# Kernel optimization log

Measured on AMD Instinct MI355X. Metric: run time of the kernel, lower is better.

The kernel has to match this reference:

```python
import jax, jax.numpy as jnp
import numpy as np

B, M, N, E, H, HID = 4, 512, 512, 256, 16, 16
D = E // H


def setup_inputs() -> dict:
    key = jax.random.key(0)
    ks = jax.random.split(key, 10)
    u = lambda k, shape, lim: jax.random.uniform(k, shape, jnp.float32, -lim, lim)
    mix1_init = (1.0 / 2.0) ** 0.5
    mix2_init = (1.0 / 16.0) ** 0.5
    return {
        "q_input": jax.random.normal(ks[0], (B, M, E), jnp.float32),
        "kv_input": jax.random.normal(ks[1], (B, N, E), jnp.float32),
        "dmat": jax.random.uniform(ks[2], (B, M, N), jnp.float32),
        "Wq": u(ks[3], (E, E), 1.0 / np.sqrt(E)),
        "Wkv": u(ks[4], (2 * E, E), 1.0 / np.sqrt(E)),
        "mix_W1": u(ks[5], (H, 2, HID), mix1_init),
        "mix_b1": u(ks[6], (H, HID), mix1_init),
        "mix_W2": u(ks[7], (H, HID, 1), mix2_init),
        "mix_b2": u(ks[8], (H, 1), mix2_init),
        "Wout": u(ks[9], (E, E), 1.0 / np.sqrt(E)),
    }


def reference(q_input, kv_input, dmat, Wq, Wkv, mix_W1, mix_b1, mix_W2, mix_b2, Wout):
    b, m, e = q_input.shape
    n = kv_input.shape[1]
    h = mix_W1.shape[0]
    d = e // h
    # projections (torch Linear: y = x @ W.T)
    q = (q_input @ Wq.T).reshape(b, m, h, d).transpose(0, 2, 1, 3)        # b h m d
    kv = (kv_input @ Wkv.T).reshape(b, n, 2, h, d)                        # (two h d) split
    k = kv[:, :, 0].transpose(0, 2, 1, 3)                                 # b h n d
    v = kv[:, :, 1].transpose(0, 2, 1, 3)                                 # b h n d
    scale = jnp.sqrt(jnp.asarray(d, q.dtype))
    scores = jnp.einsum('bhmd,bhnd->bhmn', q, k) / scale                  # b h m n
    # mix scores with dmat via per-head 2-layer MLP on the last (size-2) axis
    mix = jnp.stack([scores, jnp.broadcast_to(dmat[:, None], scores.shape)], axis=-1)  # b h m n 2
    hidden = jax.nn.relu(jnp.einsum('bhmnt,htk->bhmnk', mix, mix_W1)
                         + mix_b1[None, :, None, None, :])                # b h m n HID
    mixed = (jnp.einsum('bhmnk,hko->bhmno', hidden, mix_W2)
             + mix_b2[None, :, None, None, :])[..., 0]                    # b h m n
    probs = jax.nn.softmax(mixed, axis=-1)
    out = jnp.einsum('bhmn,bhnd->bhmd', probs, v)                         # b h m d
    out = out.transpose(0, 2, 1, 3).reshape(b, m, e)                      # b m (h d)
    return out @ Wout.T
```

## Files before the change

kernel.cpp:

```cpp
#include <hip/hip_runtime.h>
#include <stdint.h>
#include <stddef.h>

#define MM 512
#define NN 512
#define EE 256
#define HH 16
#define DD 16

typedef __bf16 bf16x8 __attribute__((ext_vector_type(8)));
typedef float f32x4 __attribute__((ext_vector_type(4)));

static __device__ __forceinline__ bf16x8 bzero8() {
  bf16x8 z;
#pragma unroll
  for (int i = 0; i < 8; ++i) z[i] = (__bf16)0.0f;
  return z;
}

static __device__ __forceinline__ bf16x8 cvt8(const float* __restrict__ p) {
  const float4 u = *(const float4*)p;
  const float4 v = *(const float4*)(p + 4);
  bf16x8 r;
  r[0] = (__bf16)u.x; r[1] = (__bf16)u.y; r[2] = (__bf16)u.z; r[3] = (__bf16)u.w;
  r[4] = (__bf16)v.x; r[5] = (__bf16)v.y; r[6] = (__bf16)v.z; r[7] = (__bf16)v.w;
  return r;
}

static __device__ __forceinline__ unsigned short f2b(float f) {
  union { __bf16 h; unsigned short u; } cv;
  cv.h = (__bf16)f;
  return cv.u;
}

static __device__ __forceinline__ float b2f(unsigned short u) {
  union { unsigned int i; float f; } cv;
  cv.i = ((unsigned int)u) << 16;
  return cv.f;
}

static __device__ __forceinline__ float b2f_lo(unsigned int u) {
  return __int_as_float((int)(u << 16));
}
static __device__ __forceinline__ float b2f_hi(unsigned int u) {
  return __int_as_float((int)(u & 0xffff0000u));
}

static __device__ __forceinline__ float fexp2(float x) {
  float r;
  asm("v_exp_f32 %0, %1" : "=v"(r) : "v"(x));
  return r;
}

static __device__ __forceinline__ unsigned int cvtpk(float lo, float hi) {
  unsigned int r;
  asm("v_cvt_pk_bf16_f32 %0, %1, %2" : "=v"(r) : "v"(lo), "v"(hi));
  return r;
}

static __device__ __forceinline__ float sload(const float* p) {
  return __int_as_float(__builtin_amdgcn_readfirstlane(__float_as_int(*p)));
}

__global__ __launch_bounds__(256) void proj_all_kernel(
    const float* __restrict__ Xq, const float* __restrict__ Xkv,
    const float* __restrict__ Wq, const float* __restrict__ Wkv,
    const float* __restrict__ Wout, const float* __restrict__ dmat,
    unsigned short* __restrict__ Qs, unsigned short* __restrict__ Ks,
    unsigned short* __restrict__ Vt,
    unsigned short* __restrict__ Whi, unsigned short* __restrict__ Wlo,
    unsigned short* __restrict__ dmatb) {
  const int by = blockIdx.y;
  const int tid = threadIdx.x;

  if (by == 13) {
    const int base = blockIdx.x * 256 + tid;
#pragma unroll
    for (int it = 0; it < 16; ++it) {
      const int i4 = it * 16384 + base;
      const float4 v = *(const float4*)(dmat + (size_t)i4 * 4);
      uint2 u;
      u.x = cvtpk(v.x, v.y);
      u.y = cvtpk(v.z, v.w);
      *(uint2*)(dmatb + (size_t)i4 * 4) = u;
    }
    return;
  }

  if (by == 12) {
    const int base = (blockIdx.x * 256 + tid) * 4;
    const float4 v = *(const float4*)(Wout + base);
    float c4[4] = {v.x, v.y, v.z, v.w};
#pragma unroll
    for (int i = 0; i < 4; ++i) {
      const unsigned short hb = f2b(c4[i]);
      Whi[base + i] = hb;
      Wlo[base + i] = f2b(c4[i] - b2f(hb));
    }
    return;
  }

  const int w = tid >> 6, l = tid & 63;
  const int lg = l >> 4, lr = l & 15;
  const int t0 = blockIdx.x * 32 + (w & 1) * 16;

  if (by < 4) {
    const int n0 = by * 64 + (w >> 1) * 32;
    f32x4 acc0 = {0.f, 0.f, 0.f, 0.f}, acc1 = {0.f, 0.f, 0.f, 0.f};
#pragma unroll
    for (int kc = 0; kc < EE; kc += 32) {
      const int k = kc + lg * 8;
      bf16x8 a  = cvt8(Xq + (size_t)(t0 + lr) * EE + k);
      bf16x8 b0 = cvt8(Wq + (size_t)(n0 + lr) * EE + k);
      bf16x8 b1 = cvt8(Wq + (size_t)(n0 + 16 + lr) * EE + k);
      acc0 = __builtin_amdgcn_mfma_f32_16x16x32_bf16(a, b0, acc0, 0, 0, 0);
      acc1 = __builtin_amdgcn_mfma_f32_16x16x32_bf16(a, b1, acc1, 0, 0, 0);
    }
#pragma unroll
    for (int r = 0; r < 4; ++r) {
      const int t = t0 + 4 * lg + r, b = t >> 9, m = t & 511;
      const int j0 = n0 + lr, j1 = j0 + 16;
      Qs[((size_t)(b * HH + (j0 >> 4)) * MM + m) * DD + (j0 & 15)] = f2b(acc0[r] * 0.25f);
      Qs[((size_t)(b * HH + (j1 >> 4)) * MM + m) * DD + (j1 & 15)] = f2b(acc1[r] * 0.25f);
    }
  } else {
    const int n0 = (by - 4) * 64 + (w >> 1) * 32;
    f32x4 acc0 = {0.f, 0.f, 0.f, 0.f}, acc1 = {0.f, 0.f, 0.f, 0.f};
#pragma unroll
    for (int kc = 0; kc < EE; kc += 32) {
      const int k = kc + lg * 8;
      bf16x8 a  = cvt8(Xkv + (size_t)(t0 + lr) * EE + k);
      bf16x8 b0 = cvt8(Wkv + (size_t)(n0 + lr) * EE + k);
      bf16x8 b1 = cvt8(Wkv + (size_t)(n0 + 16 + lr) * EE + k);
      acc0 = __builtin_amdgcn_mfma_f32_16x16x32_bf16(a, b0, acc0, 0, 0, 0);
      acc1 = __builtin_amdgcn_mfma_f32_16x16x32_bf16(a, b1, acc1, 0, 0, 0);
    }
#pragma unroll
    for (int r = 0; r < 4; ++r) {
      const int t = t0 + 4 * lg + r, b = t >> 9, n = t & 511;
#pragma unroll
      for (int fi = 0; fi < 2; ++fi) {
        const int j = n0 + lr + fi * 16;
        const float v = fi ? acc1[r] : acc0[r];
        if (j < 256) {
          Ks[((size_t)(b * HH + (j >> 4)) * NN + n) * DD + (j & 15)] = f2b(v);
        } else {
          const int jj = j - 256;
          Vt[((size_t)(b * HH + (jj >> 4)) * DD + (jj & 15)) * NN + n] = f2b(v);
        }
      }
    }
  }
}

__global__ __launch_bounds__(256, 2) void attn_kernel(
    const unsigned short* __restrict__ Qs, const unsigned short* __restrict__ Ks,
    const unsigned short* __restrict__ Vt, const unsigned short* __restrict__ dmatb,
    const float* __restrict__ W1, const float* __restrict__ b1v,
    const float* __restrict__ W2,
    unsigned short* __restrict__ Ahi, unsigned short* __restrict__ Alo) {
  __shared__ unsigned short P[32][520];
  __shared__ float red[4][32];
  float (*pvred)[2][16][16] = (float (*)[2][16][16]) & P[0][0];

  const int tid = threadIdx.x, w = tid >> 6, l = tid & 63;
  const int lg = l >> 4, lr = l & 15;
  const int bid = blockIdx.x;
  const int xcd = bid & 7, slot = bid >> 3;
  const int hh = slot & 15;
  const int g = (slot >> 4) * 8 + xcd;
  const int b = g >> 4, mt = g & 15;
  const int m0 = mt * 32;
  const int n0 = w * 128;

  const unsigned short* Qbase = Qs + ((size_t)(b * HH + hh) * MM + m0) * DD;
  const unsigned short* Kbase = Ks + (size_t)(b * HH + hh) * NN * DD;
  const unsigned short* Vbase = Vt + (size_t)(b * HH + hh) * DD * NN;
  const unsigned short* dbase = dmatb + (size_t)b * MM * NN;

  float ckv[16], bkv[16], wkp[16];
  float Ac = 0.f, Cc = 0.f;
  const float hiln2 = 0.5f * 1.4426950408889634f;
#pragma unroll
  for (int k = 0; k < 16; ++k) {
    const float ak = sload(W1 + hh * 32 + k);
    const float ck = sload(W1 + hh * 32 + 16 + k);
    const float bk = sload(b1v + hh * 16 + k);
    const float wk = hiln2 * sload(W2 + hh * 16 + k);
    Ac += wk * ak;
    Cc += wk * ck;
    const float ra = 1.0f / ak;
    ckv[k] = ck * ra;
    bkv[k] = bk * ra;
    wkp[k] = wk * fabsf(ak);
    asm volatile("" : "+v"(ckv[k]));
    asm volatile("" : "+v"(bkv[k]));
  }

  bf16x8 qb[2];
#pragma unroll
  for (int mb = 0; mb < 2; ++mb) {
    qb[mb] = bzero8();
    if (lg < 2) qb[mb] = *(const bf16x8*)(Qbase + (mb * 16 + lr) * DD + lg * 8);
  }

  const f32x4 zf = {0.f, 0.f, 0.f, 0.f};
  float psum[2] = {0.f, 0.f};

  const unsigned short* dpl0 = dbase + (size_t)(m0 + lr) * NN + n0 + 4 * lg;
  const unsigned short* dpl1 = dbase + (size_t)(m0 + 16 + lr) * NN + n0 + 4 * lg;

  uint2 dva0 = *(const uint2*)(dpl0);
  uint2 dva1 = *(const uint2*)(dpl1);
  bf16x8 ka0 = bzero8();
  if (lg < 2) ka0 = *(const bf16x8*)(Kbase + (size_t)(n0 + lr) * DD + lg * 8);

#pragma unroll
  for (int nb = 0; nb < 8; ++nb) {
    uint2 dvb0, dvb1;
    bf16x8 ka1 = bzero8();
    if (nb < 7) {
      dvb0 = *(const uint2*)(dpl0 + (nb + 1) * 16);
      dvb1 = *(const uint2*)(dpl1 + (nb + 1) * 16);
      if (lg < 2)
        ka1 = *(const bf16x8*)(Kbase + (size_t)(n0 + (nb + 1) * 16 + lr) * DD + lg * 8);
    }

    f32x4 cc[2];
    cc[0] = __builtin_amdgcn_mfma_f32_16x16x32_bf16(ka0, qb[0], zf, 0, 0, 0);
    cc[1] = __builtin_amdgcn_mfma_f32_16x16x32_bf16(ka0, qb[1], zf, 0, 0, 0);

#pragma unroll
    for (int mb = 0; mb < 2; ++mb) {
      const uint2 dvv = mb ? dva1 : dva0;
      float dunp[4];
      dunp[0] = b2f_lo(dvv.x);
      dunp[1] = b2f_hi(dvv.x);
      dunp[2] = b2f_lo(dvv.y);
      dunp[3] = b2f_hi(dvv.y);
      float ev[4];
#pragma unroll
      for (int r = 0; r < 4; ++r) {
        const float s = cc[mb][r];
        const float d = dunp[r];
        float acc = fmaf(Ac, s, Cc * d);
#pragma unroll
        for (int k = 0; k < 16; ++k) {
          const float t = fmaf(ckv[k], d, bkv[k]);
          acc = fmaf(wkp[k], fabsf(s + t), acc);
        }
        const float e = fexp2(acc);
        psum[mb] += e;
        ev[r] = e;
      }
      uint2 u;
      u.x = cvtpk(ev[0], ev[1]);
      u.y = cvtpk(ev[2], ev[3]);
      *(uint2*)&P[mb * 16 + lr][n0 + nb * 16 + 4 * lg] = u;
    }

    dva0 = dvb0;
    dva1 = dvb1;
    ka0 = ka1;
  }

#pragma unroll
  for (int mb = 0; mb < 2; ++mb) {
    psum[mb] += __shfl_xor(psum[mb], 16);
    psum[mb] += __shfl_xor(psum[mb], 32);
    if (lg == 0) red[w][mb * 16 + lr] = psum[mb];
  }

  f32x4 pv[2];
  pv[0] = zf; pv[1] = zf;
#pragma unroll
  for (int kb = 0; kb < 4; ++kb) {
    const bf16x8 vb = *(const bf16x8*)(Vbase + (size_t)lr * NN + (n0 + kb * 32 + lg * 8));
#pragma unroll
    for (int mb = 0; mb < 2; ++mb) {
      const bf16x8 pa = *(const bf16x8*)(&P[mb * 16 + lr][n0 + kb * 32 + lg * 8]);
      pv[mb] = __builtin_amdgcn_mfma_f32_16x16x32_bf16(pa, vb, pv[mb], 0, 0, 0);
    }
  }
  __syncthreads();
#pragma unroll
  for (int mb = 0; mb < 2; ++mb)
#pragma unroll
    for (int r = 0; r < 4; ++r) pvred[w][mb][4 * lg + r][lr] = pv[mb][r];
  __syncthreads();

  for (int i = tid; i < 512; i += 256) {
    const int mr = i >> 4, dd = i & 15;
    const float s = pvred[0][mr >> 4][mr & 15][dd] + pvred[1][mr >> 4][mr & 15][dd] +
                    pvred[2][mr >> 4][mr & 15][dd] + pvred[3][mr >> 4][mr & 15][dd];
    const float rs = red[0][mr] + red[1][mr] + red[2][mr] + red[3][mr];
    const float val = s / rs;
    const unsigned short hb = f2b(val);
    const size_t o = ((size_t)(b * MM) + m0 + mr) * EE + hh * DD + dd;
    Ahi[o] = hb;
    Alo[o] = f2b(val - b2f(hb));
  }
}

__global__ __launch_bounds__(256) void out_gemm_kernel(
    const unsigned short* __restrict__ Ahi, const unsigned short* __restrict__ Alo,
    const unsigned short* __restrict__ Whi, const unsigned short* __restrict__ Wlo,
    float* __restrict__ out) {
  const int tid = threadIdx.x, w = tid >> 6, l = tid & 63;
  const int lg = l >> 4, lr = l & 15;
  const int t0 = blockIdx.x * 32 + (w & 1) * 16;
  const int n0 = blockIdx.y * 64 + (w >> 1) * 32;
  f32x4 acc0 = {0.f, 0.f, 0.f, 0.f}, acc1 = {0.f, 0.f, 0.f, 0.f};
#pragma unroll
  for (int kc = 0; kc < EE; kc += 32) {
    const int k = kc + lg * 8;
    const bf16x8 ah = *(const bf16x8*)(Ahi + (size_t)(t0 + lr) * EE + k);
    const bf16x8 al = *(const bf16x8*)(Alo + (size_t)(t0 + lr) * EE + k);
    const bf16x8 bh0 = *(const bf16x8*)(Whi + (size_t)(n0 + lr) * EE + k);
    const bf16x8 bh1 = *(const bf16x8*)(Whi + (size_t)(n0 + 16 + lr) * EE + k);
    const bf16x8 bl0 = *(const bf16x8*)(Wlo + (size_t)(n0 + lr) * EE + k);
    const bf16x8 bl1 = *(const bf16x8*)(Wlo + (size_t)(n0 + 16 + lr) * EE + k);
    acc0 = __builtin_amdgcn_mfma_f32_16x16x32_bf16(ah, bh0, acc0, 0, 0, 0);
    acc0 = __builtin_amdgcn_mfma_f32_16x16x32_bf16(al, bh0, acc0, 0, 0, 0);
    acc0 = __builtin_amdgcn_mfma_f32_16x16x32_bf16(ah, bl0, acc0, 0, 0, 0);
    acc1 = __builtin_amdgcn_mfma_f32_16x16x32_bf16(ah, bh1, acc1, 0, 0, 0);
    acc1 = __builtin_amdgcn_mfma_f32_16x16x32_bf16(al, bh1, acc1, 0, 0, 0);
    acc1 = __builtin_amdgcn_mfma_f32_16x16x32_bf16(ah, bl1, acc1, 0, 0, 0);
  }
#pragma unroll
  for (int r = 0; r < 4; ++r) {
    const int row = t0 + 4 * lg + r;
    out[(size_t)row * EE + n0 + lr] = acc0[r];
    out[(size_t)row * EE + n0 + 16 + lr] = acc1[r];
  }
}

extern "C" void kernel_launch(void* const* d_in, const int* in_sizes, int n_in,
                              void* d_out, int out_size, void* d_ws, size_t ws_size,
                              hipStream_t stream) {
  const float* q_input  = (const float*)d_in[0];
  const float* kv_input = (const float*)d_in[1];
  const float* dmat     = (const float*)d_in[2];
  const float* Wq       = (const float*)d_in[3];
  const float* Wkv      = (const float*)d_in[4];
  const float* W1       = (const float*)d_in[5];
  const float* b1       = (const float*)d_in[6];
  const float* W2       = (const float*)d_in[7];
  const float* Wout     = (const float*)d_in[9];
  float* out = (float*)d_out;

  char* ws = (char*)d_ws;
  unsigned short* Qs    = (unsigned short*)(ws);
  unsigned short* Ks    = (unsigned short*)(ws + (1u << 20));
  unsigned short* Vt    = (unsigned short*)(ws + (2u << 20));
  unsigned short* Ahi   = (unsigned short*)(ws + (3u << 20));
  unsigned short* Alo   = (unsigned short*)(ws + (4u << 20));
  unsigned short* Whi   = (unsigned short*)(ws + (5u << 20));
  unsigned short* Wlo   = (unsigned short*)(ws + (5u << 20) + (1u << 17));
  unsigned short* dmatb = (unsigned short*)(ws + (6u << 20));

  proj_all_kernel<<<dim3(64, 14), 256, 0, stream>>>(q_input, kv_input, Wq, Wkv, Wout,
                                                    dmat, Qs, Ks, Vt, Whi, Wlo, dmatb);
  attn_kernel<<<dim3(1024), 256, 0, stream>>>(Qs, Ks, Vt, dmatb, W1, b1, W2,
                                              Ahi, Alo);
  out_gemm_kernel<<<dim3(64, 4), 256, 0, stream>>>(Ahi, Alo, Whi, Wlo, out);
}
```

Measured before the change: 61.81 us.

## Fuse output projection into attention kernel with atomic accumulation

Removes the separate output GEMM kernel and the Ahi/Alo workspace round trip. Each attention block multiplies its 32x16 per-head tile against the matching 16-column slice of Wout and adds the partial result into the output with float atomics, which requires zeroing the output in the projection kernel first. This saves a kernel launch and global traffic but adds 16-way atomic contention per output element, K=16 MFMAs that are half-padded with zeros, and a nondeterministic summation order.

Result: slower. 77.47 us (+25.3%).

```diff
diff --git a/kernel.cpp b/kernel.cpp
--- a/kernel.cpp
+++ b/kernel.cpp
@@ -69,9 +69,18 @@
     unsigned short* __restrict__ Qs, unsigned short* __restrict__ Ks,
     unsigned short* __restrict__ Vt,
     unsigned short* __restrict__ Whi, unsigned short* __restrict__ Wlo,
-    unsigned short* __restrict__ dmatb) {
+    unsigned short* __restrict__ dmatb, float* __restrict__ out) {
   const int by = blockIdx.y;
   const int tid = threadIdx.x;
+
+  if (by == 14) {
+    const float4 z4 = {0.f, 0.f, 0.f, 0.f};
+    const int base = blockIdx.x * 256 + tid;
+#pragma unroll
+    for (int it = 0; it < 8; ++it)
+      *(float4*)(out + (size_t)(it * 16384 + base) * 4) = z4;
+    return;
+  }
 
   if (by == 13) {
     const int base = blockIdx.x * 256 + tid;
@@ -158,10 +167,13 @@
     const unsigned short* __restrict__ Vt, const unsigned short* __restrict__ dmatb,
     const float* __restrict__ W1, const float* __restrict__ b1v,
     const float* __restrict__ W2,
-    unsigned short* __restrict__ Ahi, unsigned short* __restrict__ Alo) {
+    const unsigned short* __restrict__ Whi, const unsigned short* __restrict__ Wlo,
+    float* __restrict__ out) {
   __shared__ unsigned short P[32][520];
   __shared__ float red[4][32];
   float (*pvred)[2][16][16] = (float (*)[2][16][16]) & P[0][0];
+  unsigned short (*A_lhi)[16] = (unsigned short (*)[16]) & P[20][0];
+  unsigned short (*A_llo)[16] = (unsigned short (*)[16]) & P[22][0];
 
   const int tid = threadIdx.x, w = tid >> 6, l = tid & 63;
   const int lg = l >> 4, lr = l & 15;
@@ -296,42 +308,39 @@
     const float rs = red[0][mr] + red[1][mr] + red[2][mr] + red[3][mr];
     const float val = s / rs;
     const unsigned short hb = f2b(val);
-    const size_t o = ((size_t)(b * MM) + m0 + mr) * EE + hh * DD + dd;
-    Ahi[o] = hb;
-    Alo[o] = f2b(val - b2f(hb));
-  }
-}
-
-__global__ __launch_bounds__(256) void out_gemm_kernel(
-    const unsigned short* __restrict__ Ahi, const unsigned short* __restrict__ Alo,
-    const unsigned short* __restrict__ Whi, const unsigned short* __restrict__ Wlo,
-    float* __restrict__ out) {
-  const int tid = threadIdx.x, w = tid >> 6, l = tid & 63;
-  const int lg = l >> 4, lr = l & 15;
-  const int t0 = blockIdx.x * 32 + (w & 1) * 16;
-  const int n0 = blockIdx.y * 64 + (w >> 1) * 32;
-  f32x4 acc0 = {0.f, 0.f, 0.f, 0.f}, acc1 = {0.f, 0.f, 0.f, 0.f};
-#pragma unroll
-  for (int kc = 0; kc < EE; kc += 32) {
-    const int k = kc + lg * 8;
-    const bf16x8 ah = *(const bf16x8*)(Ahi + (size_t)(t0 + lr) * EE + k);
-    const bf16x8 al = *(const bf16x8*)(Alo + (size_t)(t0 + lr) * EE + k);
-    const bf16x8 bh0 = *(const bf16x8*)(Whi + (size_t)(n0 + lr) * EE + k);
-    const bf16x8 bh1 = *(const bf16x8*)(Whi + (size_t)(n0 + 16 + lr) * EE + k);
-    const bf16x8 bl0 = *(const bf16x8*)(Wlo + (size_t)(n0 + lr) * EE + k);
-    const bf16x8 bl1 = *(const bf16x8*)(Wlo + (size_t)(n0 + 16 + lr) * EE + k);
-    acc0 = __builtin_amdgcn_mfma_f32_16x16x32_bf16(ah, bh0, acc0, 0, 0, 0);
-    acc0 = __builtin_amdgcn_mfma_f32_16x16x32_bf16(al, bh0, acc0, 0, 0, 0);
-    acc0 = __builtin_amdgcn_mfma_f32_16x16x32_bf16(ah, bl0, acc0, 0, 0, 0);
-    acc1 = __builtin_amdgcn_mfma_f32_16x16x32_bf16(ah, bh1, acc1, 0, 0, 0);
-    acc1 = __builtin_amdgcn_mfma_f32_16x16x32_bf16(al, bh1, acc1, 0, 0, 0);
-    acc1 = __builtin_amdgcn_mfma_f32_16x16x32_bf16(ah, bl1, acc1, 0, 0, 0);
-  }
-#pragma unroll
-  for (int r = 0; r < 4; ++r) {
-    const int row = t0 + 4 * lg + r;
-    out[(size_t)row * EE + n0 + lr] = acc0[r];
-    out[(size_t)row * EE + n0 + 16 + lr] = acc1[r];
+    A_lhi[mr][dd] = hb;
+    A_llo[mr][dd] = f2b(val - b2f(hb));
+  }
+  __syncthreads();
+
+  const int c0w = w * 64;
+  const unsigned short* WhiH = Whi + hh * 16;
+  const unsigned short* WloH = Wlo + hh * 16;
+#pragma unroll
+  for (int mb = 0; mb < 2; ++mb) {
+    bf16x8 ahf = bzero8(), alf = bzero8();
+    if (lg < 2) {
+      ahf = *(const bf16x8*)&A_lhi[mb * 16 + lr][lg * 8];
+      alf = *(const bf16x8*)&A_llo[mb * 16 + lr][lg * 8];
+    }
+    f32x4 acc[4] = {zf, zf, zf, zf};
+#pragma unroll
+    for (int t = 0; t < 4; ++t) {
+      bf16x8 bh = bzero8(), bl = bzero8();
+      if (lg < 2) {
+        bh = *(const bf16x8*)(WhiH + (size_t)(c0w + t * 16 + lr) * EE + lg * 8);
+        bl = *(const bf16x8*)(WloH + (size_t)(c0w + t * 16 + lr) * EE + lg * 8);
+      }
+      acc[t] = __builtin_amdgcn_mfma_f32_16x16x32_bf16(ahf, bh, acc[t], 0, 0, 0);
+      acc[t] = __builtin_amdgcn_mfma_f32_16x16x32_bf16(alf, bh, acc[t], 0, 0, 0);
+      acc[t] = __builtin_amdgcn_mfma_f32_16x16x32_bf16(ahf, bl, acc[t], 0, 0, 0);
+    }
+    float* orow = out + ((size_t)(b * MM) + m0 + mb * 16 + 4 * lg) * EE;
+#pragma unroll
+    for (int t = 0; t < 4; ++t)
+#pragma unroll
+      for (int r = 0; r < 4; ++r)
+        atomicAdd(orow + (size_t)r * EE + c0w + t * 16 + lr, acc[t][r]);
   }
 }
 
@@ -353,15 +362,13 @@
   unsigned short* Qs    = (unsigned short*)(ws);
   unsigned short* Ks    = (unsigned short*)(ws + (1u << 20));
   unsigned short* Vt    = (unsigned short*)(ws + (2u << 20));
-  unsigned short* Ahi   = (unsigned short*)(ws + (3u << 20));
-  unsigned short* Alo   = (unsigned short*)(ws + (4u << 20));
-  unsigned short* Whi   = (unsigned short*)(ws + (5u << 20));
-  unsigned short* Wlo   = (unsigned short*)(ws + (5u << 20) + (1u << 17));
-  unsigned short* dmatb = (unsigned short*)(ws + (6u << 20));
-
-  proj_all_kernel<<<dim3(64, 14), 256, 0, stream>>>(q_input, kv_input, Wq, Wkv, Wout,
-                                                    dmat, Qs, Ks, Vt, Whi, Wlo, dmatb);
+  unsigned short* Whi   = (unsigned short*)(ws + (3u << 20));
+  unsigned short* Wlo   = (unsigned short*)(ws + (3u << 20) + (1u << 17));
+  unsigned short* dmatb = (unsigned short*)(ws + (4u << 20));
+
+  proj_all_kernel<<<dim3(64, 15), 256, 0, stream>>>(q_input, kv_input, Wq, Wkv, Wout,
+                                                    dmat, Qs, Ks, Vt, Whi, Wlo,
+                                                    dmatb, out);
   attn_kernel<<<dim3(1024), 256, 0, stream>>>(Qs, Ks, Vt, dmatb, W1, b1, W2,
-                                              Ahi, Alo);
-  out_gemm_kernel<<<dim3(64, 4), 256, 0, stream>>>(Ahi, Alo, Whi, Wlo, out);
-}
+                                              Whi, Wlo, out);
+}
```
